# Optimization experiments

Measured on AMD Instinct MI355X. Metric: run time of the kernel, lower is better.

Reference implementation:

```python
import jax, jax.numpy as jnp
import numpy as np

SCALES = (0.0625, 0.03125, 0.015625)
SIZES = ((14, 25), (7, 13), (4, 7))  # (h, w) feature sizes for 224x398 input
MODEL_H, MODEL_W = 224, 398
SCORE_THRESH = 0.05
IOU_THRESH = 0.6
TOPK = 1000


def _locations(h, w, scale):
    # FCOS grid points at stride 1/scale, centered in each cell; row-major (h, w) flatten
    ys = (jnp.arange(h, dtype=jnp.float32) + 0.5) / scale
    xs = (jnp.arange(w, dtype=jnp.float32) + 0.5) / scale
    Y, X = jnp.meshgrid(ys, xs, indexing='ij')
    return jnp.stack([X.ravel(), Y.ravel()], axis=1)  # (h*w, 2) -> (x, y)


def _decode_level(score_raw, loc_raw, ctr_raw, scale, h, w):
    # score_raw: (1,C,h,w); loc_raw: (1,4,h,w); ctr_raw: (1,1,h,w)
    s = jnp.sqrt(jax.nn.sigmoid(score_raw) * jax.nn.sigmoid(ctr_raw))[0]  # (C,h,w)
    C = s.shape[0]
    s = s.reshape(C, h * w).T                     # (hw, C)
    loc = (loc_raw[0] / scale).reshape(4, h * w).T  # (hw, 4): (l,t,r,b)
    pts = _locations(h, w, scale)
    bbox = jnp.stack([pts[:, 0] - loc[:, 0], pts[:, 1] - loc[:, 1],
                      pts[:, 0] + loc[:, 2], pts[:, 1] + loc[:, 3]], axis=1)
    return s, bbox


def _iou(b):
    area = jnp.maximum(b[:, 2] - b[:, 0], 0.0) * jnp.maximum(b[:, 3] - b[:, 1], 0.0)
    lt = jnp.maximum(b[:, None, :2], b[None, :, :2])
    rb = jnp.minimum(b[:, None, 2:], b[None, :, 2:])
    wh = jnp.maximum(rb - lt, 0.0)
    inter = wh[..., 0] * wh[..., 1]
    return inter / jnp.maximum(area[:, None] + area[None, :] - inter, 1e-9)


def _predict(heads):
    scores, bboxes = [], []
    for (sc_r, lc_r, ct_r), scale, (h, w) in zip(heads, SCALES, SIZES):
        s, b = _decode_level(sc_r, lc_r, ct_r, scale, h, w)
        scores.append(s)
        bboxes.append(b)
    score = jnp.concatenate(scores, 0)[:, 1:]  # drop background column 0
    bbox = jnp.concatenate(bboxes, 0)          # (P, 4)
    nc = score.shape[1]
    flat = score.ravel()                       # (P*nc,)
    masked = jnp.where(flat >= SCORE_THRESH, flat, -1.0)
    top_val, top_idx = jax.lax.top_k(masked, TOPK)  # sorted desc, emulates thresh+topk
    loc_idx = top_idx // nc
    label = top_idx % nc
    bx = bbox[loc_idx]                         # (TOPK, 4)
    valid = top_val >= SCORE_THRESH
    # class-aware NMS via per-class coordinate offsets (torchvision batched_nms)
    off = label.astype(bx.dtype)[:, None] * (jax.lax.stop_gradient(jnp.max(bx)) + 1.0)
    iou = _iou(bx + off)
    idx = jnp.arange(TOPK)

    def body(i, keep):
        sup = keep[i] & (iou[i] > IOU_THRESH) & (idx > i)
        return keep & (~sup)

    keep = jax.lax.fori_loop(0, TOPK, body, valid)
    # clip_boxes_to_image(bbox, size[::-1]) with size=(224,398): torchvision treats
    # (398,224) as (height,width) -> x clipped to [0,224], y clipped to [0,398]
    x1 = jnp.clip(bx[:, 0], 0.0, float(MODEL_H))
    y1 = jnp.clip(bx[:, 1], 0.0, float(MODEL_W))
    x2 = jnp.clip(bx[:, 2], 0.0, float(MODEL_H))
    y2 = jnp.clip(bx[:, 3], 0.0, float(MODEL_W))
    bx = jnp.stack([x1, y1, x2, y2], axis=1)
    # remove_small_boxes(min_size=1e-5)
    keep = keep & ((bx[:, 2] - bx[:, 0]) >= 1e-5) & ((bx[:, 3] - bx[:, 1]) >= 1e-5)
    bx = jnp.where(keep[:, None], bx, 0.0)
    sc = jnp.where(keep, top_val, -1.0)
    return bx, sc, label, keep  # padded to TOPK; keep marks valid detections


def setup_inputs() -> dict:
    key = jax.random.key(0)
    ks = jax.random.split(key, 9)
    C = 81  # class_num + background
    out = {}
    for i, (h, w) in enumerate(SIZES):
        p = f'p{i + 4}'
        out[f'score_{p}'] = jax.random.normal(ks[3 * i], (1, C, h, w), dtype=jnp.float32)
        out[f'loc_{p}'] = jax.random.uniform(ks[3 * i + 1], (1, 4, h, w), dtype=jnp.float32)
        out[f'ctr_{p}'] = jax.random.normal(ks[3 * i + 2], (1, 1, h, w), dtype=jnp.float32)
    return out


def reference(score_p4, loc_p4, ctr_p4, score_p5, loc_p5, ctr_p5,
              score_p6, loc_p6, ctr_p6):
    heads = [(score_p4, loc_p4, ctr_p4),
             (score_p5, loc_p5, ctr_p5),
             (score_p6, loc_p6, ctr_p6)]
    return _predict(heads)
```

## Files before the change

### kernel.cpp

```cpp
#include <hip/hip_runtime.h>
#include <stdint.h>

#define NLOC 469
#define NCLS 80
#define NFLAT 37520
#define TOPK 1000
#define NB 512
#define BOFF 24192
#define CAP 2048

typedef unsigned long long u64;

__device__ __forceinline__ float sigm(float x) { return 1.0f / (1.0f + expf(-x)); }

__device__ __forceinline__ uint32_t f2o(float f) {
    uint32_t u = __float_as_uint(f);
    return (u & 0x80000000u) ? ~u : (u | 0x80000000u);
}

__global__ void decode_kernel(
    const float* __restrict__ s0, const float* __restrict__ l0, const float* __restrict__ c0,
    const float* __restrict__ s1, const float* __restrict__ l1, const float* __restrict__ c1,
    const float* __restrict__ s2, const float* __restrict__ l2, const float* __restrict__ c2,
    uint32_t* __restrict__ o32, float4* __restrict__ bbox)
{
    int t = blockIdx.x * blockDim.x + threadIdx.x;
    if (t < NFLAT) {
        int p = t / NCLS;
        int k = t - p * NCLS;
        int c = k + 1;
        const float* sr; const float* cr; int local, hw;
        if (p < 350)      { sr = s0; cr = c0; local = p;       hw = 350; }
        else if (p < 441) { sr = s1; cr = c1; local = p - 350; hw = 91;  }
        else              { sr = s2; cr = c2; local = p - 441; hw = 28;  }
        float val = sqrtf(sigm(sr[c * hw + local]) * sigm(cr[local]));
        bool valid = (val >= 0.05f);
        o32[t] = valid ? f2o(val) : 0u;
    }
    if (t < NLOC) {
        int p = t;
        const float* lr; int local, hw, w; float is;
        if (p < 350)      { lr = l0; local = p;       hw = 350; w = 25; is = 16.0f; }
        else if (p < 441) { lr = l1; local = p - 350; hw = 91;  w = 13; is = 32.0f; }
        else              { lr = l2; local = p - 441; hw = 28;  w = 7;  is = 64.0f; }
        int y = local / w, x = local - y * w;
        float px = ((float)x + 0.5f) * is;
        float py = ((float)y + 0.5f) * is;
        float L = lr[local] * is;
        float T = lr[hw + local] * is;
        float R = lr[2 * hw + local] * is;
        float B = lr[3 * hw + local] * is;
        bbox[p] = make_float4(px - L, py - T, px + R, py + B);
    }
}

__global__ void __launch_bounds__(1024, 4) fused_kernel(
    const uint32_t* __restrict__ o32, const float4* __restrict__ bbox,
    float* __restrict__ out)
{
    __shared__ __align__(16) unsigned char ubuf[131072];
    int*      histW = (int*)ubuf;
    int*      histS = (int*)(ubuf + 65536);
    u64*      candL = (u64*)(ubuf + 69632);
    uint32_t* smask = (uint32_t*)ubuf;

    __shared__ float4 sboxL[TOPK];
    __shared__ float tvalL[TOPK];
    __shared__ int   tidxL[TOPK];
    __shared__ unsigned char lab8[TOPK];
    __shared__ unsigned char zrow[TOPK];
    __shared__ unsigned short csorted[TOPK];
    __shared__ int clsStart[NCLS], clsCur[NCLS];
    __shared__ uint32_t skeep32[32], validw32[32], zmaskL[32];
    __shared__ float redMax[16], redMin[16];
    __shared__ float Mp1_s;
    __shared__ int dmax_s;
    __shared__ int bstar_s;

    int tid = threadIdx.x;
    int lane = tid & 63, wv = tid >> 6;

    const int nw = (tid < 656) ? 37 : 36;
    uint32_t vbuf[37];
    #pragma unroll
    for (int k = 0; k < 37; ++k) {
        int t = tid + (k << 10);
        if (t < NFLAT) vbuf[k] = o32[t];
    }
    if (tid == 0) bstar_s = 0;
    if (tid < TOPK) { tvalL[tid] = -1.0f; tidxL[tid] = 0; }
    for (int z = tid; z < 16 * NB; z += 1024) histW[z] = 0;
    __syncthreads();
    int* myh = &histW[wv * NB];
    #pragma unroll
    for (int k = 0; k < 37; ++k) {
        if (k < nw) {
            uint32_t o = vbuf[k];
            if (o) atomicAdd(&myh[(o >> 17) - BOFF], 1);
        }
    }
    __syncthreads();
    if (tid < NB) {
        int s = 0;
        #pragma unroll
        for (int w = 0; w < 16; ++w) s += histW[w * NB + tid];
        histS[tid] = s;
    }
    __syncthreads();
    if (tid < 64) {
        int bs = NB - 8 * (tid + 1);
        int h[8];
        int s = 0;
        #pragma unroll
        for (int k = 0; k < 8; ++k) { h[k] = histS[bs + k]; s += h[k]; }
        int ws = s;
        #pragma unroll
        for (int d = 1; d < 64; d <<= 1) {
            int v = __shfl_up(ws, d, 64);
            if (tid >= d) ws += v;
        }
        int cumAbove = ws - s;
        if (cumAbove < TOPK && ws >= TOPK) {
            int running = cumAbove;
            #pragma unroll
            for (int k = 7; k >= 0; --k) {
                if (running + h[k] >= TOPK) { bstar_s = BOFF + bs + k; break; }
                running += h[k];
            }
        }
        int run = cumAbove;
        #pragma unroll
        for (int k = 7; k >= 0; --k) { histS[bs + k] = run; run += h[k]; }
    }
    __syncthreads();
    int Bstar = bstar_s;
    #pragma unroll
    for (int k = 0; k < 37; ++k) {
        if (k < nw) {
            uint32_t o = vbuf[k];
            int b = (int)(o >> 17);
            if (o && b >= Bstar) {
                int t = tid + (k << 10);
                int pos = atomicAdd(&histS[b - BOFF], 1);
                if (pos < CAP)
                    candL[pos] = ((u64)o << 32) | (u64)(0xFFFFFFFFu - (uint32_t)t);
            }
        }
    }
    __syncthreads();
    int C = min(histS[Bstar - BOFF], CAP);
    for (int p = tid; p < C; p += 1024) {
        u64 kk = candL[p];
        int bidx = (int)(kk >> 49) - BOFF;
        int segL = (bidx == NB - 1) ? 0 : min(histS[bidx + 1], CAP);
        int segR = min(histS[bidx], CAP);
        int cnt = segL;
        for (int q = segL; q < segR; ++q)
            cnt += (candL[q] > kk) ? 1 : 0;
        if (cnt < TOPK) {
            uint32_t o = (uint32_t)(kk >> 32);
            uint32_t u = (o & 0x80000000u) ? (o ^ 0x80000000u) : ~o;
            tvalL[cnt] = __uint_as_float(u);
            tidxL[cnt] = (int)(0xFFFFFFFFu - (uint32_t)(kk & 0xFFFFFFFFu));
        }
    }
    __syncthreads();

    float tvR = (tid < TOPK) ? tvalL[tid] : -1.0f;
    int   idxR = (tid < TOPK) ? tidxL[tid] : 0;
    int   pR = idxR / NCLS;
    int   labR = idxR - pR * NCLS;
    float4 bR = make_float4(0.f, 0.f, 0.f, 0.f);
    if (tid < TOPK) bR = bbox[pR];

    {
        uint4* z4 = (uint4*)smask;
        for (int z = tid; z < TOPK * 8; z += 1024) z4[z] = make_uint4(0, 0, 0, 0);
    }
    if (tid < TOPK) zrow[tid] = 0;
    float m = -3.0e38f, lmin = 3.0e38f;
    if (tid < TOPK) {
        sboxL[tid] = bR;
        lab8[tid] = (unsigned char)labR;
        m = fmaxf(fmaxf(bR.x, bR.y), fmaxf(bR.z, bR.w));
        lmin = fminf(bR.x, bR.y);
    }
    for (int o = 32; o > 0; o >>= 1) {
        m = fmaxf(m, __shfl_down(m, o, 64));
        lmin = fminf(lmin, __shfl_down(lmin, o, 64));
    }
    if (lane == 0) { redMax[wv] = m; redMin[wv] = lmin; }
    if (tid < NCLS) clsCur[tid] = 0;
    __syncthreads();
    if (tid == 0) {
        float mm = redMax[0], ll = redMin[0];
        for (int q = 1; q < 16; ++q) { mm = fmaxf(mm, redMax[q]); ll = fminf(ll, redMin[q]); }
        float Mp1 = mm + 1.0f;
        Mp1_s = Mp1;
        int dm = 79;
        if (Mp1 > 0.0f) {
            float ratio = (mm - ll) / Mp1;
            dm = (int)ceilf(ratio);
            if (dm < 0) dm = 0;
            if (dm > 79) dm = 79;
        }
        dmax_s = dm;
    }
    __syncthreads();
    float Mp1 = Mp1_s;
    if (tid < TOPK) {
        float off = (float)labR * Mp1;
        sboxL[tid] = make_float4(bR.x + off, bR.y + off, bR.z + off, bR.w + off);
        atomicAdd(&clsCur[labR], 1);
    }
    __syncthreads();
    if (tid < 64) {
        int l = tid;
        int e0 = clsCur[l];
        int e1 = (l < 16) ? clsCur[64 + l] : 0;
        int s = e0;
        for (int d = 1; d < 64; d <<= 1) {
            int v = __shfl_up(s, d, 64);
            if (l >= d) s += v;
        }
        int tot64 = __shfl(s, 63, 64);
        int s2 = e1;
        for (int d = 1; d < 16; d <<= 1) {
            int v = __shfl_up(s2, d, 64);
            if (l >= d) s2 += v;
        }
        int ex0 = s - e0;
        clsStart[l] = ex0;
        clsCur[l] = ex0;
        if (l < 16) {
            int ex1 = tot64 + s2 - e1;
            clsStart[64 + l] = ex1;
            clsCur[64 + l] = ex1;
        }
    }
    __syncthreads();
    if (tid < TOPK) {
        int pos = atomicAdd(&clsCur[labR], 1);
        csorted[pos] = (unsigned short)tid;
    }
    __syncthreads();
    if (tid < TOPK) {
        int s = tid;
        int i = csorted[s];
        int c = lab8[i];
        float4 si = sboxL[i];
        float ai = fmaxf(si.z - si.x, 0.f) * fmaxf(si.w - si.y, 0.f);
        int chi = c + dmax_s; if (chi > NCLS - 1) chi = NCLS - 1;
        int endPos = clsCur[chi];
        for (int t = s + 1; t < endPos; ++t) {
            int j = csorted[t];
            float4 sj = sboxL[j];
            float aj = fmaxf(sj.z - sj.x, 0.f) * fmaxf(sj.w - sj.y, 0.f);
            float ltx = fmaxf(si.x, sj.x), lty = fmaxf(si.y, sj.y);
            float rbx = fminf(si.z, sj.z), rby = fminf(si.w, sj.w);
            float iw = fmaxf(rbx - ltx, 0.f), ih = fmaxf(rby - lty, 0.f);
            float inter = iw * ih;
            float iou = inter / fmaxf(ai + aj - inter, 1e-9f);
            if (iou > 0.6f) {
                int lo = min(i, j), hi = max(i, j);
                atomicOr(&smask[lo * 32 + (hi >> 5)], 1u << (hi & 31));
                zrow[lo] = 1;
            }
        }
    }
    __syncthreads();
    {
        u64 zb = __ballot(tid < TOPK && zrow[tid] != 0);
        if (lane == 0) {
            zmaskL[wv * 2]     = (uint32_t)zb;
            zmaskL[wv * 2 + 1] = (uint32_t)(zb >> 32);
        }
        u64 bal = __ballot(tid < TOPK && tvR >= 0.05f);
        if (lane == 0) {
            validw32[wv * 2]     = (uint32_t)bal;
            validw32[wv * 2 + 1] = (uint32_t)(bal >> 32);
        }
    }
    __syncthreads();
    if (tid < 32) {
        const int ln = tid;
        uint32_t vwreg = validw32[ln];
        uint32_t zreg  = zmaskL[ln];
        uint32_t sup = 0;
        for (int wc = 0; wc < 32; ++wc) {
            uint32_t nzw = (uint32_t)__builtin_amdgcn_readlane((int)zreg, wc);
            uint32_t avail = (uint32_t)__builtin_amdgcn_readlane((int)vwreg, wc)
                           & ~(uint32_t)__builtin_amdgcn_readlane((int)sup, wc);
            int p0 = -1, p1 = -1, p2 = -1;
            uint32_t R0 = 0, R1 = 0, R2 = 0;
            if (nzw) { p0 = __ffs(nzw) - 1; nzw &= nzw - 1;
                       R0 = smask[(wc * 32 + p0) * 32 + ln]; }
            if (nzw) { p1 = __ffs(nzw) - 1; nzw &= nzw - 1;
                       R1 = smask[(wc * 32 + p1) * 32 + ln]; }
            if (nzw) { p2 = __ffs(nzw) - 1; nzw &= nzw - 1;
                       R2 = smask[(wc * 32 + p2) * 32 + ln]; }
            while (p0 >= 0) {
                uint32_t rc = (uint32_t)__builtin_amdgcn_readlane((int)R0, wc);
                uint32_t kp = (avail >> p0) & 1u;
                uint32_t mm = 0u - kp;
                sup   |= R0 & mm;
                avail &= ~(rc & mm);
                p0 = p1; R0 = R1; p1 = p2; R1 = R2;
                if (nzw) { p2 = __ffs(nzw) - 1; nzw &= nzw - 1;
                           R2 = smask[(wc * 32 + p2) * 32 + ln]; }
                else p2 = -1;
            }
            if (ln == 0) skeep32[wc] = avail;
        }
    }
    __syncthreads();
    if (tid < TOPK) {
        bool kp = (skeep32[tid >> 5] >> (tid & 31)) & 1u;
        float x1 = fminf(fmaxf(bR.x, 0.f), 224.f);
        float y1 = fminf(fmaxf(bR.y, 0.f), 398.f);
        float x2 = fminf(fmaxf(bR.z, 0.f), 224.f);
        float y2 = fminf(fmaxf(bR.w, 0.f), 398.f);
        kp = kp && ((x2 - x1) >= 1e-5f) && ((y2 - y1) >= 1e-5f);
        out[tid * 4 + 0] = kp ? x1 : 0.f;
        out[tid * 4 + 1] = kp ? y1 : 0.f;
        out[tid * 4 + 2] = kp ? x2 : 0.f;
        out[tid * 4 + 3] = kp ? y2 : 0.f;
        out[4 * TOPK + tid] = kp ? tvR : -1.0f;
        out[5 * TOPK + tid] = (float)labR;
        out[6 * TOPK + tid] = kp ? 1.0f : 0.0f;
    }
}

extern "C" void kernel_launch(void* const* d_in, const int* in_sizes, int n_in,
                              void* d_out, int out_size, void* d_ws, size_t ws_size,
                              hipStream_t stream)
{
    const float* s0 = (const float*)d_in[0];
    const float* l0 = (const float*)d_in[1];
    const float* c0 = (const float*)d_in[2];
    const float* s1 = (const float*)d_in[3];
    const float* l1 = (const float*)d_in[4];
    const float* c1 = (const float*)d_in[5];
    const float* s2 = (const float*)d_in[6];
    const float* l2 = (const float*)d_in[7];
    const float* c2 = (const float*)d_in[8];

    uint8_t* ws = (uint8_t*)d_ws;
    uint32_t* o32  = (uint32_t*)(ws);
    float4*   bbox = (float4*)  (ws + 150080);

    decode_kernel<<<dim3((NFLAT + 255) / 256), 256, 0, stream>>>(
        s0, l0, c0, s1, l1, c1, s2, l2, c2, o32, bbox);
    fused_kernel<<<1, 1024, 0, stream>>>(o32, bbox, (float*)d_out);
}
```

Measured before the change: 46.20 us.

## Split radix-select histogram and scatter into multi-block kernels before NMS

Moves the histogram build into the decode kernel with per-block shared histograms, adds a single-block kernel that reduces the histograms and finds the threshold bucket, and a multi-block scatter kernel that writes candidates to global memory. The single-block NMS kernel then only loads the prepared candidates. This spreads the serial single-block pass over 37k values across many CUs, at the cost of two extra kernel launches and global round-trips. The NMS kernel also reads all CAP candidate slots, including unwritten ones beyond the count.

```diff
diff --git a/kernel.cpp b/kernel.cpp
--- a/kernel.cpp
+++ b/kernel.cpp
@@ -8,6 +8,7 @@
 #define NB 512
 #define BOFF 24192
 #define CAP 2048
+#define NBLK 147
 
 typedef unsigned long long u64;
 
@@ -22,9 +23,13 @@
     const float* __restrict__ s0, const float* __restrict__ l0, const float* __restrict__ c0,
     const float* __restrict__ s1, const float* __restrict__ l1, const float* __restrict__ c1,
     const float* __restrict__ s2, const float* __restrict__ l2, const float* __restrict__ c2,
-    uint32_t* __restrict__ o32, float4* __restrict__ bbox)
-{
-    int t = blockIdx.x * blockDim.x + threadIdx.x;
+    uint32_t* __restrict__ o32, float4* __restrict__ bbox, int* __restrict__ histP)
+{
+    __shared__ int histL[NB];
+    int tid = threadIdx.x;
+    int t = blockIdx.x * 256 + tid;
+    histL[tid] = 0; histL[tid + 256] = 0;
+    __syncthreads();
     if (t < NFLAT) {
         int p = t / NCLS;
         int k = t - p * NCLS;
@@ -35,7 +40,9 @@
         else              { sr = s2; cr = c2; local = p - 441; hw = 28;  }
         float val = sqrtf(sigm(sr[c * hw + local]) * sigm(cr[local]));
         bool valid = (val >= 0.05f);
-        o32[t] = valid ? f2o(val) : 0u;
+        uint32_t o = valid ? f2o(val) : 0u;
+        o32[t] = o;
+        if (o) atomicAdd(&histL[(int)(o >> 17) - BOFF], 1);
     }
     if (t < NLOC) {
         int p = t;
@@ -52,16 +59,78 @@
         float B = lr[3 * hw + local] * is;
         bbox[p] = make_float4(px - L, py - T, px + R, py + B);
     }
-}
-
-__global__ void __launch_bounds__(1024, 4) fused_kernel(
-    const uint32_t* __restrict__ o32, const float4* __restrict__ bbox,
+    __syncthreads();
+    int* hp = &histP[blockIdx.x * NB];
+    hp[tid] = histL[tid];
+    hp[tid + 256] = histL[tid + 256];
+}
+
+__global__ void __launch_bounds__(512) select_kernel(
+    const int* __restrict__ histP, int* __restrict__ cursG, int* __restrict__ bstarG)
+{
+    __shared__ int histS[NB];
+    __shared__ int bstar_s;
+    int tid = threadIdx.x;
+    if (tid == 0) bstar_s = 0;
+    int s = 0;
+    for (int w = 0; w < NBLK; ++w) s += histP[w * NB + tid];
+    histS[tid] = s;
+    __syncthreads();
+    if (tid < 64) {
+        int bs = NB - 8 * (tid + 1);
+        int h[8];
+        int sum = 0;
+        #pragma unroll
+        for (int k = 0; k < 8; ++k) { h[k] = histS[bs + k]; sum += h[k]; }
+        int ws = sum;
+        #pragma unroll
+        for (int d = 1; d < 64; d <<= 1) {
+            int v = __shfl_up(ws, d, 64);
+            if (tid >= d) ws += v;
+        }
+        int cumAbove = ws - sum;
+        if (cumAbove < TOPK && ws >= TOPK) {
+            int running = cumAbove;
+            #pragma unroll
+            for (int k = 7; k >= 0; --k) {
+                if (running + h[k] >= TOPK) { bstar_s = BOFF + bs + k; break; }
+                running += h[k];
+            }
+        }
+        int run = cumAbove;
+        #pragma unroll
+        for (int k = 7; k >= 0; --k) { histS[bs + k] = run; run += h[k]; }
+    }
+    __syncthreads();
+    cursG[tid] = histS[tid];
+    if (tid == 0) bstarG[0] = bstar_s;
+}
+
+__global__ void scatter_kernel(
+    const uint32_t* __restrict__ o32, const int* __restrict__ bstarG,
+    int* __restrict__ cursG, u64* __restrict__ candG)
+{
+    int t = blockIdx.x * 256 + threadIdx.x;
+    int Bstar = bstarG[0];
+    if (t < NFLAT) {
+        uint32_t o = o32[t];
+        int b = (int)(o >> 17);
+        if (o && b >= Bstar) {
+            int pos = atomicAdd(&cursG[b - BOFF], 1);
+            if (pos < CAP)
+                candG[pos] = ((u64)o << 32) | (u64)(0xFFFFFFFFu - (uint32_t)t);
+        }
+    }
+}
+
+__global__ void __launch_bounds__(1024, 4) nms_kernel(
+    const int* __restrict__ cursG, const int* __restrict__ bstarG,
+    const u64* __restrict__ candG, const float4* __restrict__ bbox,
     float* __restrict__ out)
 {
     __shared__ __align__(16) unsigned char ubuf[131072];
-    int*      histW = (int*)ubuf;
-    int*      histS = (int*)(ubuf + 65536);
-    u64*      candL = (u64*)(ubuf + 69632);
+    int*      histS = (int*)ubuf;
+    u64*      candL = (u64*)(ubuf + 4096);
     uint32_t* smask = (uint32_t*)ubuf;
 
     __shared__ float4 sboxL[TOPK];
@@ -75,79 +144,20 @@
     __shared__ float redMax[16], redMin[16];
     __shared__ float Mp1_s;
     __shared__ int dmax_s;
-    __shared__ int bstar_s;
 
     int tid = threadIdx.x;
     int lane = tid & 63, wv = tid >> 6;
 
-    const int nw = (tid < 656) ? 37 : 36;
-    uint32_t vbuf[37];
-    #pragma unroll
-    for (int k = 0; k < 37; ++k) {
-        int t = tid + (k << 10);
-        if (t < NFLAT) vbuf[k] = o32[t];
-    }
-    if (tid == 0) bstar_s = 0;
+    if (tid < NB) histS[tid] = cursG[tid];
+    {
+        u64 c0v = candG[tid];
+        u64 c1v = candG[tid + 1024];
+        candL[tid] = c0v;
+        candL[tid + 1024] = c1v;
+    }
     if (tid < TOPK) { tvalL[tid] = -1.0f; tidxL[tid] = 0; }
-    for (int z = tid; z < 16 * NB; z += 1024) histW[z] = 0;
-    __syncthreads();
-    int* myh = &histW[wv * NB];
-    #pragma unroll
-    for (int k = 0; k < 37; ++k) {
-        if (k < nw) {
-            uint32_t o = vbuf[k];
-            if (o) atomicAdd(&myh[(o >> 17) - BOFF], 1);
-        }
-    }
-    __syncthreads();
-    if (tid < NB) {
-        int s = 0;
-        #pragma unroll
-        for (int w = 0; w < 16; ++w) s += histW[w * NB + tid];
-        histS[tid] = s;
-    }
-    __syncthreads();
-    if (tid < 64) {
-        int bs = NB - 8 * (tid + 1);
-        int h[8];
-        int s = 0;
-        #pragma unroll
-        for (int k = 0; k < 8; ++k) { h[k] = histS[bs + k]; s += h[k]; }
-        int ws = s;
-        #pragma unroll
-        for (int d = 1; d < 64; d <<= 1) {
-            int v = __shfl_up(ws, d, 64);
-            if (tid >= d) ws += v;
-        }
-        int cumAbove = ws - s;
-        if (cumAbove < TOPK && ws >= TOPK) {
-            int running = cumAbove;
-            #pragma unroll
-            for (int k = 7; k >= 0; --k) {
-                if (running + h[k] >= TOPK) { bstar_s = BOFF + bs + k; break; }
-                running += h[k];
-            }
-        }
-        int run = cumAbove;
-        #pragma unroll
-        for (int k = 7; k >= 0; --k) { histS[bs + k] = run; run += h[k]; }
-    }
-    __syncthreads();
-    int Bstar = bstar_s;
-    #pragma unroll
-    for (int k = 0; k < 37; ++k) {
-        if (k < nw) {
-            uint32_t o = vbuf[k];
-            int b = (int)(o >> 17);
-            if (o && b >= Bstar) {
-                int t = tid + (k << 10);
-                int pos = atomicAdd(&histS[b - BOFF], 1);
-                if (pos < CAP)
-                    candL[pos] = ((u64)o << 32) | (u64)(0xFFFFFFFFu - (uint32_t)t);
-            }
-        }
-    }
-    __syncthreads();
+    __syncthreads();
+    int Bstar = bstarG[0];
     int C = min(histS[Bstar - BOFF], CAP);
     for (int p = tid; p < C; p += 1024) {
         u64 kk = candL[p];
@@ -346,10 +356,16 @@
     const float* c2 = (const float*)d_in[8];
 
     uint8_t* ws = (uint8_t*)d_ws;
-    uint32_t* o32  = (uint32_t*)(ws);
-    float4*   bbox = (float4*)  (ws + 150080);
-
-    decode_kernel<<<dim3((NFLAT + 255) / 256), 256, 0, stream>>>(
-        s0, l0, c0, s1, l1, c1, s2, l2, c2, o32, bbox);
-    fused_kernel<<<1, 1024, 0, stream>>>(o32, bbox, (float*)d_out);
-}
+    uint32_t* o32   = (uint32_t*)(ws);
+    float4*   bbox  = (float4*)  (ws + 150080);
+    int*      histP = (int*)     (ws + 157584);
+    int*      cursG = (int*)     (ws + 458640);
+    int*      bstarG= (int*)     (ws + 460688);
+    u64*      candG = (u64*)     (ws + 460704);
+
+    decode_kernel<<<dim3(NBLK), 256, 0, stream>>>(
+        s0, l0, c0, s1, l1, c1, s2, l2, c2, o32, bbox, histP);
+    select_kernel<<<1, 512, 0, stream>>>(histP, cursG, bstarG);
+    scatter_kernel<<<dim3(NBLK), 256, 0, stream>>>(o32, bstarG, cursG, candG);
+    nms_kernel<<<1, 1024, 0, stream>>>(cursG, bstarG, candG, bbox, (float*)d_out);
+}
```

Result: slower. 54.97 us (+19.0%).

## Build score histogram in parallel decode blocks instead of single fused block

Applied to the files above, without the earlier changes.

Each decode block now builds a 512-bin shared-memory histogram of its encoded scores and writes it as a per-block partial to workspace. The single-block fused kernel sums the 147 partials per bin instead of running its own per-wave atomic histogram over all 37520 values. This moves serial work out of the one-block stage into the wide grid. In exchange it adds global partial writes and a 147-iteration global-load reduction per bin.

```diff
diff --git a/kernel.cpp b/kernel.cpp
--- a/kernel.cpp
+++ b/kernel.cpp
@@ -8,6 +8,7 @@
 #define NB 512
 #define BOFF 24192
 #define CAP 2048
+#define NBLK 147
 
 typedef unsigned long long u64;
 
@@ -22,9 +23,13 @@
     const float* __restrict__ s0, const float* __restrict__ l0, const float* __restrict__ c0,
     const float* __restrict__ s1, const float* __restrict__ l1, const float* __restrict__ c1,
     const float* __restrict__ s2, const float* __restrict__ l2, const float* __restrict__ c2,
-    uint32_t* __restrict__ o32, float4* __restrict__ bbox)
+    uint32_t* __restrict__ o32, float4* __restrict__ bbox, int* __restrict__ histP)
 {
-    int t = blockIdx.x * blockDim.x + threadIdx.x;
+    __shared__ int histL[NB];
+    int tid = threadIdx.x;
+    int t = blockIdx.x * 256 + tid;
+    histL[tid] = 0; histL[tid + 256] = 0;
+    __syncthreads();
     if (t < NFLAT) {
         int p = t / NCLS;
         int k = t - p * NCLS;
@@ -35,7 +40,9 @@
         else              { sr = s2; cr = c2; local = p - 441; hw = 28;  }
         float val = sqrtf(sigm(sr[c * hw + local]) * sigm(cr[local]));
         bool valid = (val >= 0.05f);
-        o32[t] = valid ? f2o(val) : 0u;
+        uint32_t o = valid ? f2o(val) : 0u;
+        o32[t] = o;
+        if (o) atomicAdd(&histL[(int)(o >> 17) - BOFF], 1);
     }
     if (t < NLOC) {
         int p = t;
@@ -52,16 +59,19 @@
         float B = lr[3 * hw + local] * is;
         bbox[p] = make_float4(px - L, py - T, px + R, py + B);
     }
+    __syncthreads();
+    int* hp = &histP[blockIdx.x * NB];
+    hp[tid] = histL[tid];
+    hp[tid + 256] = histL[tid + 256];
 }
 
 __global__ void __launch_bounds__(1024, 4) fused_kernel(
-    const uint32_t* __restrict__ o32, const float4* __restrict__ bbox,
-    float* __restrict__ out)
+    const uint32_t* __restrict__ o32, const int* __restrict__ histP,
+    const float4* __restrict__ bbox, float* __restrict__ out)
 {
     __shared__ __align__(16) unsigned char ubuf[131072];
-    int*      histW = (int*)ubuf;
-    int*      histS = (int*)(ubuf + 65536);
-    u64*      candL = (u64*)(ubuf + 69632);
+    int*      histS = (int*)ubuf;
+    u64*      candL = (u64*)(ubuf + 4096);
     uint32_t* smask = (uint32_t*)ubuf;
 
     __shared__ float4 sboxL[TOPK];
@@ -89,21 +99,9 @@
     }
     if (tid == 0) bstar_s = 0;
     if (tid < TOPK) { tvalL[tid] = -1.0f; tidxL[tid] = 0; }
-    for (int z = tid; z < 16 * NB; z += 1024) histW[z] = 0;
-    __syncthreads();
-    int* myh = &histW[wv * NB];
-    #pragma unroll
-    for (int k = 0; k < 37; ++k) {
-        if (k < nw) {
-            uint32_t o = vbuf[k];
-            if (o) atomicAdd(&myh[(o >> 17) - BOFF], 1);
-        }
-    }
-    __syncthreads();
     if (tid < NB) {
         int s = 0;
-        #pragma unroll
-        for (int w = 0; w < 16; ++w) s += histW[w * NB + tid];
+        for (int w = 0; w < NBLK; ++w) s += histP[w * NB + tid];
         histS[tid] = s;
     }
     __syncthreads();
@@ -346,10 +344,11 @@
     const float* c2 = (const float*)d_in[8];
 
     uint8_t* ws = (uint8_t*)d_ws;
-    uint32_t* o32  = (uint32_t*)(ws);
-    float4*   bbox = (float4*)  (ws + 150080);
-
-    decode_kernel<<<dim3((NFLAT + 255) / 256), 256, 0, stream>>>(
-        s0, l0, c0, s1, l1, c1, s2, l2, c2, o32, bbox);
-    fused_kernel<<<1, 1024, 0, stream>>>(o32, bbox, (float*)d_out);
+    uint32_t* o32   = (uint32_t*)(ws);
+    float4*   bbox  = (float4*)  (ws + 150080);
+    int*      histP = (int*)     (ws + 157584);
+
+    decode_kernel<<<dim3(NBLK), 256, 0, stream>>>(
+        s0, l0, c0, s1, l1, c1, s2, l2, c2, o32, bbox, histP);
+    fused_kernel<<<1, 1024, 0, stream>>>(o32, histP, bbox, (float*)d_out);
 }
```

New measurement: 49.15 us. +6.4%, slower.

## Fuse decode into the single-block selection kernel, keep boxes in LDS

Applied to the files above, without the earlier changes.

Merges the decode kernel into the single-block top-k/NMS kernel. Each of the 1024 threads now computes its 37 sigmoid/sqrt scores directly from the inputs, and the 469 boxes are built into shared memory, so the workspace round trip and the second launch go away. The cost is that the decode work, previously spread over about 147 blocks, now runs serially within one workgroup. A barrier is added before the shared buffer region holding the boxes is reused.

```diff
diff --git a/kernel.cpp b/kernel.cpp
--- a/kernel.cpp
+++ b/kernel.cpp
@@ -18,50 +18,17 @@
     return (u & 0x80000000u) ? ~u : (u | 0x80000000u);
 }
 
-__global__ void decode_kernel(
+__global__ void __launch_bounds__(1024, 4) mono_kernel(
     const float* __restrict__ s0, const float* __restrict__ l0, const float* __restrict__ c0,
     const float* __restrict__ s1, const float* __restrict__ l1, const float* __restrict__ c1,
     const float* __restrict__ s2, const float* __restrict__ l2, const float* __restrict__ c2,
-    uint32_t* __restrict__ o32, float4* __restrict__ bbox)
-{
-    int t = blockIdx.x * blockDim.x + threadIdx.x;
-    if (t < NFLAT) {
-        int p = t / NCLS;
-        int k = t - p * NCLS;
-        int c = k + 1;
-        const float* sr; const float* cr; int local, hw;
-        if (p < 350)      { sr = s0; cr = c0; local = p;       hw = 350; }
-        else if (p < 441) { sr = s1; cr = c1; local = p - 350; hw = 91;  }
-        else              { sr = s2; cr = c2; local = p - 441; hw = 28;  }
-        float val = sqrtf(sigm(sr[c * hw + local]) * sigm(cr[local]));
-        bool valid = (val >= 0.05f);
-        o32[t] = valid ? f2o(val) : 0u;
-    }
-    if (t < NLOC) {
-        int p = t;
-        const float* lr; int local, hw, w; float is;
-        if (p < 350)      { lr = l0; local = p;       hw = 350; w = 25; is = 16.0f; }
-        else if (p < 441) { lr = l1; local = p - 350; hw = 91;  w = 13; is = 32.0f; }
-        else              { lr = l2; local = p - 441; hw = 28;  w = 7;  is = 64.0f; }
-        int y = local / w, x = local - y * w;
-        float px = ((float)x + 0.5f) * is;
-        float py = ((float)y + 0.5f) * is;
-        float L = lr[local] * is;
-        float T = lr[hw + local] * is;
-        float R = lr[2 * hw + local] * is;
-        float B = lr[3 * hw + local] * is;
-        bbox[p] = make_float4(px - L, py - T, px + R, py + B);
-    }
-}
-
-__global__ void __launch_bounds__(1024, 4) fused_kernel(
-    const uint32_t* __restrict__ o32, const float4* __restrict__ bbox,
     float* __restrict__ out)
 {
     __shared__ __align__(16) unsigned char ubuf[131072];
     int*      histW = (int*)ubuf;
     int*      histS = (int*)(ubuf + 65536);
     u64*      candL = (u64*)(ubuf + 69632);
+    float4*   bboxL = (float4*)(ubuf + 86016);
     uint32_t* smask = (uint32_t*)ubuf;
 
     __shared__ float4 sboxL[TOPK];
@@ -84,8 +51,34 @@
     uint32_t vbuf[37];
     #pragma unroll
     for (int k = 0; k < 37; ++k) {
+        vbuf[k] = 0u;
         int t = tid + (k << 10);
-        if (t < NFLAT) vbuf[k] = o32[t];
+        if (t < NFLAT) {
+            int p = t / NCLS;
+            int kk = t - p * NCLS;
+            int c = kk + 1;
+            const float* sr; const float* cr; int local, hw;
+            if (p < 350)      { sr = s0; cr = c0; local = p;       hw = 350; }
+            else if (p < 441) { sr = s1; cr = c1; local = p - 350; hw = 91;  }
+            else              { sr = s2; cr = c2; local = p - 441; hw = 28;  }
+            float val = sqrtf(sigm(sr[c * hw + local]) * sigm(cr[local]));
+            if (val >= 0.05f) vbuf[k] = f2o(val);
+        }
+    }
+    if (tid < NLOC) {
+        int p = tid;
+        const float* lr; int local, hw, w; float is;
+        if (p < 350)      { lr = l0; local = p;       hw = 350; w = 25; is = 16.0f; }
+        else if (p < 441) { lr = l1; local = p - 350; hw = 91;  w = 13; is = 32.0f; }
+        else              { lr = l2; local = p - 441; hw = 28;  w = 7;  is = 64.0f; }
+        int y = local / w, x = local - y * w;
+        float px = ((float)x + 0.5f) * is;
+        float py = ((float)y + 0.5f) * is;
+        float L = lr[local] * is;
+        float T = lr[hw + local] * is;
+        float R = lr[2 * hw + local] * is;
+        float B = lr[3 * hw + local] * is;
+        bboxL[p] = make_float4(px - L, py - T, px + R, py + B);
     }
     if (tid == 0) bstar_s = 0;
     if (tid < TOPK) { tvalL[tid] = -1.0f; tidxL[tid] = 0; }
@@ -171,7 +164,8 @@
     int   pR = idxR / NCLS;
     int   labR = idxR - pR * NCLS;
     float4 bR = make_float4(0.f, 0.f, 0.f, 0.f);
-    if (tid < TOPK) bR = bbox[pR];
+    if (tid < TOPK) bR = bboxL[pR];
+    __syncthreads();
 
     {
         uint4* z4 = (uint4*)smask;
@@ -345,11 +339,6 @@
     const float* l2 = (const float*)d_in[7];
     const float* c2 = (const float*)d_in[8];
 
-    uint8_t* ws = (uint8_t*)d_ws;
-    uint32_t* o32  = (uint32_t*)(ws);
-    float4*   bbox = (float4*)  (ws + 150080);
-
-    decode_kernel<<<dim3((NFLAT + 255) / 256), 256, 0, stream>>>(
-        s0, l0, c0, s1, l1, c1, s2, l2, c2, o32, bbox);
-    fused_kernel<<<1, 1024, 0, stream>>>(o32, bbox, (float*)d_out);
+    mono_kernel<<<1, 1024, 0, stream>>>(
+        s0, l0, c0, s1, l1, c1, s2, l2, c2, (float*)d_out);
 }
```

Measured after the change: 65.07 us. 1.41x slower.
